# Kernel tuning notes

Measured on AMD Instinct MI355X. Metric: run time of the kernel, lower is better.

The kernel has to match this reference:

```python
import jax, jax.numpy as jnp
import numpy as np

# MORRConfig_20um_MQ (all-pass MRR) constants used by mrr_roundtrip_phase_to_tr(intensity=True)
A = 0.987   # attenuation_factor a
R = 0.99    # coupling_factor r
KS, STRIDE, PAD = 3, 1, 1
IN_C, OUT_C, MB = 32, 64, 8


def _unfold(x, ks, pad, stride):
    # torch.nn.functional.unfold: output channel order is (C, kh, kw), C slowest
    B, C, H, W = x.shape
    xp = jnp.pad(x, ((0, 0), (0, 0), (pad, pad), (pad, pad)))
    Ho = (H + 2 * pad - ks) // stride + 1
    Wo = (W + 2 * pad - ks) // stride + 1
    cols = jnp.stack(
        [xp[:, :, i:i + stride * Ho:stride, j:j + stride * Wo:stride]
         for i in range(ks) for j in range(ks)],
        axis=2,
    )  # [B, C, ks*ks, Ho, Wo]
    return cols.reshape(B, C * ks * ks, Ho * Wo), Ho, Wo


def _mrr_tr(phase):
    # all-pass MRR intensity transmission vs roundtrip phase detuning
    c = jnp.cos(phase)
    return (A * A - 2.0 * A * R * c + R * R) / (1.0 - 2.0 * A * R * c + (A * R) ** 2)


def setup_inputs() -> dict:
    key = jax.random.key(0)
    k1, k2, k3 = jax.random.split(key, 3)
    B, H, W = 8, 64, 64
    wic = IN_C * KS * KS           # 288, divisible by miniblock -> no zero pad
    q = wic // MB                  # grid_dim_x = 36
    p = OUT_C // MB                # grid_dim_y = 8
    x = jax.random.normal(k1, (B, IN_C, H, W), jnp.float32)
    weight = jax.random.normal(k2, (p, q, MB), jnp.float32)
    morr_output_scale = jax.random.normal(k3, (max(1, q // 2) + 1,), jnp.float32)
    return {"x": x, "weight": weight, "morr_output_scale": morr_output_scale}


def reference(x, weight, morr_output_scale):
    B = x.shape[0]
    p, q, k = weight.shape
    w = jnp.abs(weight)                                  # w_bit=16 -> build_weight() = |W|
    cols, Ho, Wo = _unfold(x, KS, PAD, STRIDE)           # [B, wic, L]
    xf = cols.transpose(0, 2, 1).reshape(-1, q, k)       # [N, q, k], N = B*Ho*Wo
    xf = xf * xf                                         # intensity modulation x^2
    # block-circulant matvec via rFFT (circular convolution per (p, q) block)
    Xf = jnp.fft.rfft(xf, n=k, axis=-1)                  # [N, q, kf]
    Wf = jnp.fft.rfft(w, n=k, axis=-1)                   # [p, q, kf]
    phase = jnp.fft.irfft(Xf[:, None, :, :] * Wf[None, :, :, :], n=k, axis=-1)  # [N, p, q, k]
    tr = _mrr_tr(phase)                                  # MORR nonlinear transfer
    # differential-rail output scale (even grid_dim_x branch)
    s = morr_output_scale
    if q % 2 == 0:
        scale = jnp.concatenate([s[:-1], -s[:-1]])
    else:
        scale = jnp.concatenate([s[:-1], s[-1:], -s[:-1]])
    out = jnp.einsum('npqk,q->npk', tr, scale).reshape(-1, p * k)[:, :OUT_C]
    return out.reshape(B, Ho, Wo, OUT_C).transpose(0, 3, 1, 2)  # [B, OUT_C, Ho, Wo]
```

## Files before the change

kernel.cpp:

```cpp
#include <hip/hip_runtime.h>
#include <math.h>
#include <utility>


template <class F, size_t... I>
__device__ __forceinline__ void sf_impl(F&& f, std::index_sequence<I...>) {
    (f(std::integral_constant<size_t, I>{}), ...);
}
template <size_t N, class F>
__device__ __forceinline__ void static_for(F&& f) {
    sf_impl(f, std::make_index_sequence<N>{});
}

__global__ __launch_bounds__(1024, 4)
void morr_kernel(const float* __restrict__ xg, const float* __restrict__ wg,
                 const float* __restrict__ sg, float* __restrict__ out) {
    __shared__ __align__(16) float lds_x[32 * 10 * 24];
    __shared__ __align__(16) float lds_w[8 * 36 * 8];
    __shared__ float lds_nds[36];

    constexpr double Ad = 0.987, Rd = 0.99;
    constexpr float K2 = (float)(2.0 * Ad * Rd);
    constexpr float C2 = (float)(1.0 + (Ad * Rd) * (Ad * Rd));
    constexpr float D  = (float)((1.0 - Ad * Ad) * (1.0 - Rd * Rd));
    constexpr float INV2PI = 0.15915494309189535f;

    const int tid = threadIdx.x;
    const int b  = blockIdx.z;
    const int tr = blockIdx.y;
    const int tc = blockIdx.x;
    const int gr0 = tr * 8, gc0 = tc * 16;

    for (int i = tid; i < 32 * 10 * 18; i += 1024) {
        int c = i / 180, rem = i - c * 180;
        int r = rem / 18, cl = rem - r * 18;
        int gr = gr0 - 1 + r, gc = gc0 - 1 + cl;
        float v = 0.f;
        if ((unsigned)gr < 64u && (unsigned)gc < 64u)
            v = xg[((b * 32 + c) * 64 + gr) * 64 + gc];
        lds_x[c * 240 + r * 24 + cl] = v * v;
    }
    for (int i = tid; i < 2304; i += 1024) lds_w[i] = fabsf(wg[i]) * INV2PI;
    if (tid < 36) {
        float sv = (tid < 18) ? sg[tid] : -sg[tid - 18];
        lds_nds[tid] = -D * sv;
    }
    __syncthreads();

    const int px  = tid & 127;
    const int p   = tid >> 7;
    const int row = px >> 4;
    const int col = px & 15;

    const float* __restrict__ xb = &lds_x[row * 24 + col];
    const float* __restrict__ wb = &lds_w[p * 288];

    float acc[8];
    static_for<8>([&](auto T) { acc[T] = 0.f; });

    for (int cb = 0; cb < 4; ++cb) {
        const float* __restrict__ xcb = xb + cb * 1920;
        const float* __restrict__ wcb = wb + cb * 72;
        const float* __restrict__ ncb = &lds_nds[cb * 9];

        static_for<9>([&](auto QQ) {
            constexpr int qq = QQ;
            float xq[8];
            static_for<8>([&](auto S) {
                constexpr int s  = S;
                constexpr int u  = qq * 8 + s;
                constexpr int off = (u / 9) * 240 + ((u % 9) / 3) * 24 + (u % 3);
                xq[s] = xcb[off];
            });
            const float nds = ncb[qq];
            const float4 wa = *reinterpret_cast<const float4*>(wcb + qq * 8);
            const float4 wz = *reinterpret_cast<const float4*>(wcb + qq * 8 + 4);
            const float wv[8] = {wa.x, wa.y, wa.z, wa.w, wz.x, wz.y, wz.z, wz.w};

            static_for<8>([&](auto T) {
                constexpr int t = T;
                float ph = xq[0] * wv[t];
                static_for<7>([&](auto S) {
                    constexpr int s = (int)S + 1;
                    ph = fmaf(xq[s], wv[(t - s + 8) & 7], ph);
                });
                float cv  = __builtin_amdgcn_cosf(ph);
                float den = fmaf(-K2, cv, C2);
                float inv = __builtin_amdgcn_rcpf(den);
                acc[t] = fmaf(nds, inv, acc[t]);
            });
        });
    }

    const int gr = gr0 + row, gc = gc0 + col;
    static_for<8>([&](auto T) {
        constexpr int t = T;
        const int oc = p * 8 + t;
        out[(b * 64 + oc) * 4096 + gr * 64 + gc] = acc[t];
    });
}

extern "C" void kernel_launch(void* const* d_in, const int* in_sizes, int n_in,
                              void* d_out, int out_size, void* d_ws, size_t ws_size,
                              hipStream_t stream) {
    const float* x = (const float*)d_in[0];
    const float* w = (const float*)d_in[1];
    const float* s = (const float*)d_in[2];
    float* out = (float*)d_out;
    dim3 grid(4, 8, 8);
    dim3 block(1024);
    hipLaunchKernelGGL(morr_kernel, grid, block, 0, stream, x, w, s, out);
}
```

Before: 90.12 us.

## Split q-reduction across wave halves and halve spatial tile to double blocks

Shrinks each block's spatial tile from 8x16 to 8x8 pixels and doubles the grid. Within a wave, the two 32-lane halves now each handle half of the q channel blocks, and the partial sums are combined with a cross-lane shuffle. The aim is more blocks to fill the GPU's compute units and higher occupancy, with launch bounds raised to 8. In exchange, halo reloads per output grow, the LDS row stride changes to 40 (which may affect bank conflicts), and each thread writes only 4 of the 8 outputs.

Result: slower. 116.1 us (+28.8%).

```diff
diff --git a/kernel.cpp b/kernel.cpp
--- a/kernel.cpp
+++ b/kernel.cpp
@@ -12,10 +12,10 @@
     sf_impl(f, std::make_index_sequence<N>{});
 }
 
-__global__ __launch_bounds__(1024, 4)
+__global__ __launch_bounds__(1024, 8)
 void morr_kernel(const float* __restrict__ xg, const float* __restrict__ wg,
                  const float* __restrict__ sg, float* __restrict__ out) {
-    __shared__ __align__(16) float lds_x[32 * 10 * 24];
+    __shared__ __align__(16) float lds_x[32 * 10 * 40];
     __shared__ __align__(16) float lds_w[8 * 36 * 8];
     __shared__ float lds_nds[36];
 
@@ -26,19 +26,18 @@
     constexpr float INV2PI = 0.15915494309189535f;
 
     const int tid = threadIdx.x;
-    const int b  = blockIdx.z;
-    const int tr = blockIdx.y;
-    const int tc = blockIdx.x;
-    const int gr0 = tr * 8, gc0 = tc * 16;
+    const int b   = blockIdx.z;
+    const int gr0 = blockIdx.y * 8;
+    const int gc0 = blockIdx.x * 8;
 
-    for (int i = tid; i < 32 * 10 * 18; i += 1024) {
-        int c = i / 180, rem = i - c * 180;
-        int r = rem / 18, cl = rem - r * 18;
+    for (int i = tid; i < 3200; i += 1024) {
+        int c = i / 100, rem = i - c * 100;
+        int r = rem / 10, cl = rem - r * 10;
         int gr = gr0 - 1 + r, gc = gc0 - 1 + cl;
         float v = 0.f;
         if ((unsigned)gr < 64u && (unsigned)gc < 64u)
             v = xg[((b * 32 + c) * 64 + gr) * 64 + gc];
-        lds_x[c * 240 + r * 24 + cl] = v * v;
+        lds_x[c * 400 + r * 40 + cl] = v * v;
     }
     for (int i = tid; i < 2304; i += 1024) lds_w[i] = fabsf(wg[i]) * INV2PI;
     if (tid < 36) {
@@ -47,29 +46,32 @@
     }
     __syncthreads();
 
-    const int px  = tid & 127;
     const int p   = tid >> 7;
-    const int row = px >> 4;
-    const int col = px & 15;
+    const int pxh = (tid >> 6) & 1;
+    const int qh  = (tid >> 5) & 1;
+    const int pxl = tid & 31;
+    const int row = pxh * 4 + (pxl >> 3);
+    const int col = pxl & 7;
 
-    const float* __restrict__ xb = &lds_x[row * 24 + col];
-    const float* __restrict__ wb = &lds_w[p * 288];
+    const float* __restrict__ xb = &lds_x[row * 40 + col];
+    const float* __restrict__ wp = &lds_w[p * 288];
 
     float acc[8];
     static_for<8>([&](auto T) { acc[T] = 0.f; });
 
-    for (int cb = 0; cb < 4; ++cb) {
-        const float* __restrict__ xcb = xb + cb * 1920;
-        const float* __restrict__ wcb = wb + cb * 72;
+    for (int cbl = 0; cbl < 2; ++cbl) {
+        const int cb = qh * 2 + cbl;
+        const float* __restrict__ xcb = xb + cb * 3200;
+        const float* __restrict__ wcb = wp + cb * 72;
         const float* __restrict__ ncb = &lds_nds[cb * 9];
 
         static_for<9>([&](auto QQ) {
             constexpr int qq = QQ;
             float xq[8];
             static_for<8>([&](auto S) {
-                constexpr int s  = S;
-                constexpr int u  = qq * 8 + s;
-                constexpr int off = (u / 9) * 240 + ((u % 9) / 3) * 24 + (u % 3);
+                constexpr int s   = S;
+                constexpr int u   = qq * 8 + s;
+                constexpr int off = (u / 9) * 400 + ((u % 9) / 3) * 40 + (u % 3);
                 xq[s] = xcb[off];
             });
             const float nds = ncb[qq];
@@ -92,11 +94,18 @@
         });
     }
 
-    const int gr = gr0 + row, gc = gc0 + col;
+    float accF[8];
     static_for<8>([&](auto T) {
         constexpr int t = T;
+        accF[t] = acc[t] + __shfl_xor(acc[t], 32);
+    });
+
+    const int gr = gr0 + row, gc = gc0 + col;
+    static_for<4>([&](auto TT) {
+        constexpr int tt = TT;
+        const int t  = (qh << 2) + tt;
         const int oc = p * 8 + t;
-        out[(b * 64 + oc) * 4096 + gr * 64 + gc] = acc[t];
+        out[(b * 64 + oc) * 4096 + gr * 64 + gc] = accF[t];
     });
 }
 
@@ -107,7 +116,7 @@
     const float* w = (const float*)d_in[1];
     const float* s = (const float*)d_in[2];
     float* out = (float*)d_out;
-    dim3 grid(4, 8, 8);
+    dim3 grid(8, 8, 8);
     dim3 block(1024);
     hipLaunchKernelGGL(morr_kernel, grid, block, 0, stream, x, w, s, out);
 }
```
